# Kernel tuning notes

Hardware: AMD Instinct MI355X
Metric: run time of the kernel (lower is better)

The kernel has to match this reference:

```python
import jax, jax.numpy as jnp
import numpy as np

NEG_SLOPE = 0.2

def gat_conv(x, src, dst, n, W, a_src, a_dst, b):
    # PyG GATConv, heads=1: h = xW; e_ij = LeakyReLU(a_src.h_j + a_dst.h_i)
    # alpha = softmax over incoming edges of i; out_i = sum_j alpha_ij * h_j + b
    h = x @ W                               # [N, F_out]
    s_src = h @ a_src                       # [N]
    s_dst = h @ a_dst                       # [N]
    e = s_src[src] + s_dst[dst]             # [E]
    e = jnp.where(e > 0, e, NEG_SLOPE * e)  # leaky relu
    # numerically stable scatter-softmax over destination groups
    m = jax.ops.segment_max(e, dst, num_segments=n)          # [N]
    ee = jnp.exp(e - m[dst])                                  # [E]
    denom = jax.ops.segment_sum(ee, dst, num_segments=n)      # [N]
    alpha = ee / denom[dst]                                    # [E]
    out = jax.ops.segment_sum(alpha[:, None] * h[src], dst, num_segments=n)
    return out + b

def add_self_loops(edge_index, n):
    loops = jnp.arange(n, dtype=edge_index.dtype)
    src = jnp.concatenate([edge_index[0], loops])
    dst = jnp.concatenate([edge_index[1], loops])
    return src, dst

def setup_inputs() -> dict:
    key = jax.random.key(0)
    ks = jax.random.split(key, 12)
    N, E, F_IN, H1, H2, C = 50000, 800000, 1433, 512, 256, 7
    x = jax.random.normal(ks[0], (N, F_IN), dtype=jnp.float32)
    edge_index = jax.random.randint(ks[1], (2, E), 0, N, dtype=jnp.int64)
    def glorot(k, shape):
        lim = float(np.sqrt(6.0 / (shape[0] + shape[-1])))
        return jax.random.uniform(k, shape, jnp.float32, -lim, lim)
    params = {
        'W1': glorot(ks[2], (F_IN, H1)), 'as1': glorot(ks[3], (H1,)), 'ad1': glorot(ks[4], (H1,)), 'b1': jnp.zeros((H1,), jnp.float32),
        'W2': glorot(ks[5], (H1, H2)), 'as2': glorot(ks[6], (H2,)), 'ad2': glorot(ks[7], (H2,)), 'b2': jnp.zeros((H2,), jnp.float32),
        'W3': glorot(ks[8], (H2, C)), 'as3': glorot(ks[9], (C,)), 'ad3': glorot(ks[10], (C,)), 'b3': jnp.zeros((C,), jnp.float32),
    }
    return {'x': x, 'edge_index': edge_index, **params}

def reference(x, edge_index, W1, as1, ad1, b1, W2, as2, ad2, b2, W3, as3, ad3, b3):
    n = x.shape[0]
    src, dst = add_self_loops(edge_index, n)
    h = jax.nn.relu(gat_conv(x, src, dst, n, W1, as1, ad1, b1))
    h = jax.nn.relu(gat_conv(h, src, dst, n, W2, as2, ad2, b2))
    h = gat_conv(h, src, dst, n, W3, as3, ad3, b3)
    return jax.nn.log_softmax(h, axis=1)
```

## Files before the change

### kernel.cpp

```cpp
#include <hip/hip_runtime.h>
#include <hip/hip_bf16.h>
#include <math.h>

constexpr int N_NODES = 50000;
constexpr int E_EDGES = 800000;
constexpr int E_TOT   = E_EDGES + N_NODES;
constexpr int F_IN  = 1433;
constexpr int KPAD1 = 1440;
constexpr int F1 = 512;
constexpr int F2 = 256;
constexpr int NC = 7;
constexpr int MAXDEG = 1024;
constexpr float NEG_SLOPE = 0.2f;

typedef unsigned short u16;
typedef unsigned int   u32;
typedef short s16x8 __attribute__((ext_vector_type(8)));
typedef float f32x4 __attribute__((ext_vector_type(4)));
typedef float float4a __attribute__((ext_vector_type(4), aligned(4)));

__device__ inline u16 f2b(float f) {
    u32 u = __float_as_uint(f);
    u32 r = (u + 0x7fffu + ((u >> 16) & 1u)) >> 16;
    return (u16)r;
}
__device__ inline float b2f(u16 b) { return __uint_as_float(((u32)b) << 16); }

__device__ inline u32 pkbf16(float lo, float hi) {
    union { __hip_bfloat162 h; u32 u; } c;
    c.h = __float22bfloat162_rn(make_float2(lo, hi));
    return c.u;
}

__device__ inline void gload_lds16(const void* g, void* l) {
    __builtin_amdgcn_global_load_lds(
        (const __attribute__((address_space(1))) u32*)g,
        (__attribute__((address_space(3))) u32*)l, 16, 0, 0);
}

__global__ void count_dst_kernel(const int* __restrict__ dst, int* __restrict__ counts) {
    int i = blockIdx.x * blockDim.x + threadIdx.x;
    if (i < E_TOT) {
        int d = (i < E_EDGES) ? dst[i] : (i - E_EDGES);
        atomicAdd(&counts[d], 1);
    }
}

__global__ __launch_bounds__(1024) void scan_kernel(const int* __restrict__ counts,
                                                    int* __restrict__ row_ptr, int n) {
    __shared__ int part[1024];
    int t = threadIdx.x;
    int chunk = (n + 1023) / 1024;
    int lo = t * chunk;
    int hi = min(lo + chunk, n);
    int s = 0;
    for (int i = lo; i < hi; ++i) s += counts[i];
    part[t] = s;
    __syncthreads();
    for (int off = 1; off < 1024; off <<= 1) {
        int v = 0;
        if (t >= off) v = part[t - off];
        __syncthreads();
        part[t] += v;
        __syncthreads();
    }
    int run = part[t] - s;
    for (int i = lo; i < hi; ++i) { row_ptr[i] = run; run += counts[i]; }
    if (t == 1023) row_ptr[n] = part[1023];
}

__global__ void scatter_kernel(const int* __restrict__ src, const int* __restrict__ dst,
                               const int* __restrict__ row_ptr, int* __restrict__ fill,
                               int* __restrict__ col) {
    int i = blockIdx.x * blockDim.x + threadIdx.x;
    if (i < E_TOT) {
        int s = (i < E_EDGES) ? src[i] : (i - E_EDGES);
        int d = (i < E_EDGES) ? dst[i] : (i - E_EDGES);
        int p = row_ptr[d] + atomicAdd(&fill[d], 1);
        col[p] = s;
    }
}

__global__ void convert_wt_kernel(const float* __restrict__ W, u32* __restrict__ Wt,
                                  int K, int Nn, int KP) {
    int p = blockIdx.x * blockDim.x + threadIdx.x;
    int ppr = KP / 2;
    if (p >= Nn * ppr) return;
    int n = p / ppr;
    int k = (p - n * ppr) * 2;
    float v0 = (k + 0 < K) ? W[(size_t)(k + 0) * Nn + n] : 0.f;
    float v1 = (k + 1 < K) ? W[(size_t)(k + 1) * Nn + n] : 0.f;
    Wt[p] = (u32)f2b(v0) | ((u32)f2b(v1) << 16);
}

#define GEMM1_COMPUTE(P)                                                        \
    {                                                                           \
        const u16* sAc = &sA[(P) * ABUF];                                       \
        const u16* sBc = &sB[(P) * BBUF];                                       \
        s16x8 af[4], bf[8];                                                     \
        _Pragma("unroll")                                                       \
        for (int mt = 0; mt < 4; ++mt)                                          \
            af[mt] = *(const s16x8*)&sAc[(mt * 16 + lm) * 32 + rdoff];          \
        _Pragma("unroll")                                                       \
        for (int nt = 0; nt < 8; ++nt)                                          \
            bf[nt] = *(const s16x8*)&sBc[(wave * 128 + nt * 16 + lm) * 32 + rdoff]; \
        _Pragma("unroll")                                                       \
        for (int mt = 0; mt < 4; ++mt)                                          \
            _Pragma("unroll")                                                   \
            for (int nt = 0; nt < 8; ++nt)                                      \
                acc[mt][nt] = __builtin_amdgcn_mfma_f32_16x16x32_bf16(          \
                    af[mt], bf[nt], acc[mt][nt], 0, 0, 0);                      \
    }

#define GEMM1_BODY(i, P, Q)                                                     \
    {                                                                           \
        __builtin_amdgcn_s_barrier();                                           \
        int kA = ((i) + 2) * 32;                                                \
        aR0[P] = *(const float4a*)(xcol + kA);                                  \
        aR1[P] = *(const float4a*)(xcol + kA + 4);                              \
        int kB = ((i) + 1) * 32;                                                \
        _Pragma("unroll")                                                       \
        for (int c = 0; c < 8; ++c) gload_lds16(gB[c] + kB, lB[c] + (Q) * BBUF);\
        asm volatile("s_waitcnt vmcnt(10)" ::: "memory");                       \
        GEMM1_COMPUTE(P);                                                       \
        uint4 pk_;                                                              \
        pk_.x = pkbf16(aR0[Q][0], aR0[Q][1]);                                   \
        pk_.y = pkbf16(aR0[Q][2], aR0[Q][3]);                                   \
        pk_.z = pkbf16(aR1[Q][0], aR1[Q][1]);                                   \
        pk_.w = pkbf16(aR1[Q][2], aR1[Q][3]);                                   \
        *(uint4*)&sA[(Q) * ABUF + tid * 8] = pk_;                               \
        asm volatile("s_waitcnt lgkmcnt(0)" ::: "memory");                      \
    }

__global__ __launch_bounds__(256, 2) void gemm1_fused(const float* __restrict__ A,
                                                      const u16* __restrict__ Bt,
                                                      u16* __restrict__ C) {
    constexpr int M = N_NODES;
    constexpr int ABUF = 64 * 32;
    constexpr int BBUF = 512 * 32;
    __shared__ u16 sA[2 * ABUF];
    __shared__ u16 sB[2 * BBUF];
    int tid  = threadIdx.x;
    int wave = tid >> 6;
    int lane = tid & 63;
    int quad = lane >> 4;
    int lm   = lane & 15;
    int m0 = blockIdx.x * 64;

    int arow  = min(m0 + (tid >> 2), M - 1);
    int aslot = (tid & 3) ^ ((tid >> 3) & 3);
    const float* xcol = A + (size_t)arow * F_IN + aslot * 8;

    const u16* gB[8];
    u16* lB[8];
#pragma unroll
    for (int c = 0; c < 8; ++c) {
        int chunk = wave * 8 + c;
        int row  = chunk * 16 + (lane >> 2);
        int slot = (lane & 3) ^ ((lane >> 3) & 3);
        gB[c] = Bt + (size_t)row * KPAD1 + slot * 8;
        lB[c] = &sB[chunk * 512];
    }

    f32x4 acc[4][8];
#pragma unroll
    for (int i = 0; i < 4; ++i)
#pragma unroll
        for (int j = 0; j < 8; ++j) acc[i][j] = (f32x4){0.f, 0.f, 0.f, 0.f};

    int rdoff = (quad ^ ((lm >> 1) & 3)) * 8;

    float4a aR0[2], aR1[2];

    aR0[0] = *(const float4a*)(xcol + 0);
    aR1[0] = *(const float4a*)(xcol + 4);
    aR0[1] = *(const float4a*)(xcol + 32);
    aR1[1] = *(const float4a*)(xcol + 36);
#pragma unroll
    for (int c = 0; c < 8; ++c) gload_lds16(gB[c], lB[c]);
    asm volatile("s_waitcnt vmcnt(10)" ::: "memory");
    {
        uint4 pk_;
        pk_.x = pkbf16(aR0[0][0], aR0[0][1]);
        pk_.y = pkbf16(aR0[0][2], aR0[0][3]);
        pk_.z = pkbf16(aR1[0][0], aR1[0][1]);
        pk_.w = pkbf16(aR1[0][2], aR1[0][3]);
        *(uint4*)&sA[tid * 8] = pk_;
    }
    asm volatile("s_waitcnt lgkmcnt(0)" ::: "memory");

    for (int ii = 0; ii < 42; ii += 2) {
        GEMM1_BODY(ii, 0, 1);
        GEMM1_BODY(ii + 1, 1, 0);
    }

    __syncthreads();
    float tv[8];
    {
        int c0 = 1408 + aslot * 8;
#pragma unroll
        for (int q = 0; q < 8; ++q)
            tv[q] = (c0 + q < F_IN) ? xcol[1408 + q] : 0.f;
    }
#pragma unroll
    for (int c = 0; c < 8; ++c) gload_lds16(gB[c] + 43 * 32, lB[c] + BBUF);
    GEMM1_COMPUTE(0);
    {
        uint4 pk_;
        pk_.x = pkbf16(aR0[1][0], aR0[1][1]);
        pk_.y = pkbf16(aR0[1][2], aR0[1][3]);
        pk_.z = pkbf16(aR1[1][0], aR1[1][1]);
        pk_.w = pkbf16(aR1[1][2], aR1[1][3]);
        *(uint4*)&sA[ABUF + tid * 8] = pk_;
    }
    __syncthreads();
#pragma unroll
    for (int c = 0; c < 8; ++c) gload_lds16(gB[c] + 44 * 32, lB[c]);
    GEMM1_COMPUTE(1);
    {
        uint4 pk_;
        pk_.x = pkbf16(tv[0], tv[1]);
        pk_.y = pkbf16(tv[2], tv[3]);
        pk_.z = pkbf16(tv[4], tv[5]);
        pk_.w = pkbf16(tv[6], tv[7]);
        *(uint4*)&sA[tid * 8] = pk_;
    }
    __syncthreads();
    GEMM1_COMPUTE(0);

#pragma unroll
    for (int mt = 0; mt < 4; ++mt) {
        int mbase = m0 + mt * 16 + quad * 4;
#pragma unroll
        for (int nt = 0; nt < 8; ++nt) {
            int n = wave * 128 + nt * 16 + lm;
#pragma unroll
            for (int r = 0; r < 4; ++r) {
                int m = mbase + r;
                if (m < M) C[(size_t)m * F1 + n] = f2b(acc[mt][nt][r]);
            }
        }
    }
}

__global__ __launch_bounds__(256) void mfma_gemm_bt(const u16* __restrict__ A,
                                                    const u16* __restrict__ Bt,
                                                    u16* __restrict__ C,
                                                    int M, int N, int K) {
    __shared__ u16 sA[128 * 32];
    __shared__ u16 sB[128 * 32];
    int tid  = threadIdx.x;
    int wave = tid >> 6;
    int lane = tid & 63;
    int quad = lane >> 4;
    int lm   = lane & 15;
    int wm = wave & 1;
    int wn = wave >> 1;
    int m0 = blockIdx.y * 128;
    int n0 = blockIdx.x * 128;

    int ch0 = wave * 2, ch1 = wave * 2 + 1;
    int rsub = lane >> 2;
    int slot = (lane & 3) ^ ((lane >> 3) & 3);
    int csub = slot * 8;
    int ar0 = min(m0 + ch0 * 16 + rsub, M - 1);
    int ar1 = min(m0 + ch1 * 16 + rsub, M - 1);
    int br0 = n0 + ch0 * 16 + rsub;
    int br1 = n0 + ch1 * 16 + rsub;
    const u16* gA0 = A + (size_t)ar0 * K + csub;
    const u16* gA1 = A + (size_t)ar1 * K + csub;
    const u16* gB0 = Bt + (size_t)br0 * K + csub;
    const u16* gB1 = Bt + (size_t)br1 * K + csub;

    f32x4 acc[4][4];
#pragma unroll
    for (int i = 0; i < 4; ++i)
#pragma unroll
        for (int j = 0; j < 4; ++j) acc[i][j] = (f32x4){0.f, 0.f, 0.f, 0.f};

    int rdoff = (quad ^ ((lm >> 1) & 3)) * 8;

    for (int k0 = 0; k0 < K; k0 += 32) {
        gload_lds16(gA0 + k0, &sA[ch0 * 512]);
        gload_lds16(gA1 + k0, &sA[ch1 * 512]);
        gload_lds16(gB0 + k0, &sB[ch0 * 512]);
        gload_lds16(gB1 + k0, &sB[ch1 * 512]);
        __syncthreads();

        s16x8 af[4], bf[4];
#pragma unroll
        for (int mt = 0; mt < 4; ++mt)
            af[mt] = *(const s16x8*)&sA[(wm * 64 + mt * 16 + lm) * 32 + rdoff];
#pragma unroll
        for (int nt = 0; nt < 4; ++nt)
            bf[nt] = *(const s16x8*)&sB[(wn * 64 + nt * 16 + lm) * 32 + rdoff];
#pragma unroll
        for (int mt = 0; mt < 4; ++mt)
#pragma unroll
            for (int nt = 0; nt < 4; ++nt)
                acc[mt][nt] = __builtin_amdgcn_mfma_f32_16x16x32_bf16(
                    af[mt], bf[nt], acc[mt][nt], 0, 0, 0);
        __syncthreads();
    }

#pragma unroll
    for (int mt = 0; mt < 4; ++mt) {
        int mbase = m0 + wm * 64 + mt * 16 + quad * 4;
#pragma unroll
        for (int nt = 0; nt < 4; ++nt) {
            int n = n0 + wn * 64 + nt * 16 + lm;
#pragma unroll
            for (int r = 0; r < 4; ++r) {
                int m = mbase + r;
                if (m < M) C[(size_t)m * N + n] = f2b(acc[mt][nt][r]);
            }
        }
    }
}

template <int F>
__global__ __launch_bounds__(256) void scores_bf16_kernel(const u16* __restrict__ h,
                                                          const float* __restrict__ a_src,
                                                          const float* __restrict__ a_dst,
                                                          float* __restrict__ s_src,
                                                          float* __restrict__ s_dst, int n) {
    int gwid = (blockIdx.x * blockDim.x + threadIdx.x) >> 6;
    int lane = threadIdx.x & 63;
    if (gwid >= n) return;
    const u32* row = (const u32*)(h + (size_t)gwid * F);
    float acc1 = 0.f, acc2 = 0.f;
    for (int p = lane; p < F / 2; p += 64) {
        u32 u = row[p];
        float v0 = b2f((u16)(u & 0xffff));
        float v1 = b2f((u16)(u >> 16));
        acc1 += v0 * a_src[2 * p] + v1 * a_src[2 * p + 1];
        acc2 += v0 * a_dst[2 * p] + v1 * a_dst[2 * p + 1];
    }
#pragma unroll
    for (int o = 32; o; o >>= 1) {
        acc1 += __shfl_xor(acc1, o);
        acc2 += __shfl_xor(acc2, o);
    }
    if (lane == 0) { s_src[gwid] = acc1; s_dst[gwid] = acc2; }
}

template <int F>
__global__ __launch_bounds__(256) void scores_kernel(const float* __restrict__ h,
                                                     const float* __restrict__ a_src,
                                                     const float* __restrict__ a_dst,
                                                     float* __restrict__ s_src,
                                                     float* __restrict__ s_dst, int n) {
    int gwid = (blockIdx.x * blockDim.x + threadIdx.x) >> 6;
    int lane = threadIdx.x & 63;
    if (gwid >= n) return;
    const float* row = h + (size_t)gwid * F;
    float acc1 = 0.f, acc2 = 0.f;
    for (int f = lane; f < F; f += 64) {
        float v = row[f];
        acc1 += v * a_src[f];
        acc2 += v * a_dst[f];
    }
#pragma unroll
    for (int o = 32; o; o >>= 1) {
        acc1 += __shfl_xor(acc1, o);
        acc2 += __shfl_xor(acc2, o);
    }
    if (lane == 0) { s_src[gwid] = acc1; s_dst[gwid] = acc2; }
}

template <int F, bool OUT_BF16>
__global__ __launch_bounds__(256) void agg_online_kernel(
        const u16* __restrict__ h, const float* __restrict__ s_src,
        const float* __restrict__ s_dst, const float* __restrict__ bias,
        const int* __restrict__ row_ptr, const int* __restrict__ col,
        void* __restrict__ out, int n) {
    constexpr int UPL = F / 128;
    int gwid = (blockIdx.x * blockDim.x + threadIdx.x) >> 6;
    int lane = threadIdx.x & 63;
    if (gwid >= n) return;
    int beg = row_ptr[gwid];
    int end = row_ptr[gwid + 1];
    float sd = s_dst[gwid];
    const u32* hw = (const u32*)h;
    int loff = lane * UPL;

    float m = -1e30f, denom = 0.f;
    float acc[2 * UPL];
#pragma unroll
    for (int e = 0; e < 2 * UPL; ++e) acc[e] = 0.f;

    int j = beg;
    for (; j + 2 <= end; j += 2) {
        int c0 = col[j], c1 = col[j + 1];
        const u32* r0 = hw + (size_t)c0 * (F / 2) + loff;
        const u32* r1 = hw + (size_t)c1 * (F / 2) + loff;
        u32 v0[UPL], v1[UPL];
        if constexpr (UPL == 4) {
            uint4 q0 = *(const uint4*)r0; v0[0]=q0.x; v0[1]=q0.y; v0[2]=q0.z; v0[3]=q0.w;
            uint4 q1 = *(const uint4*)r1; v1[0]=q1.x; v1[1]=q1.y; v1[2]=q1.z; v1[3]=q1.w;
        } else {
            uint2 q0 = *(const uint2*)r0; v0[0]=q0.x; v0[1]=q0.y;
            uint2 q1 = *(const uint2*)r1; v1[0]=q1.x; v1[1]=q1.y;
        }
        float e0 = s_src[c0] + sd; e0 = (e0 > 0.f) ? e0 : NEG_SLOPE * e0;
        float e1 = s_src[c1] + sd; e1 = (e1 > 0.f) ? e1 : NEG_SLOPE * e1;
        float mn = fmaxf(fmaxf(m, e0), e1);
        float sc = expf(m - mn);
        float w0 = expf(e0 - mn);
        float w1 = expf(e1 - mn);
        denom = denom * sc + w0 + w1;
        m = mn;
#pragma unroll
        for (int u = 0; u < UPL; ++u) {
            acc[2*u]   = acc[2*u]   * sc + w0 * b2f((u16)(v0[u] & 0xffff))
                                         + w1 * b2f((u16)(v1[u] & 0xffff));
            acc[2*u+1] = acc[2*u+1] * sc + w0 * b2f((u16)(v0[u] >> 16))
                                         + w1 * b2f((u16)(v1[u] >> 16));
        }
    }
    if (j < end) {
        int c0 = col[j];
        const u32* r0 = hw + (size_t)c0 * (F / 2) + loff;
        u32 v0[UPL];
        if constexpr (UPL == 4) {
            uint4 q0 = *(const uint4*)r0; v0[0]=q0.x; v0[1]=q0.y; v0[2]=q0.z; v0[3]=q0.w;
        } else {
            uint2 q0 = *(const uint2*)r0; v0[0]=q0.x; v0[1]=q0.y;
        }
        float e0 = s_src[c0] + sd; e0 = (e0 > 0.f) ? e0 : NEG_SLOPE * e0;
        float mn = fmaxf(m, e0);
        float sc = expf(m - mn);
        float w0 = expf(e0 - mn);
        denom = denom * sc + w0;
        m = mn;
#pragma unroll
        for (int u = 0; u < UPL; ++u) {
            acc[2*u]   = acc[2*u]   * sc + w0 * b2f((u16)(v0[u] & 0xffff));
            acc[2*u+1] = acc[2*u+1] * sc + w0 * b2f((u16)(v0[u] >> 16));
        }
    }

    float inv = 1.0f / denom;
    if constexpr (OUT_BF16) {
        const float2* bp2 = (const float2*)bias;
        u32 ov[UPL];
#pragma unroll
        for (int u = 0; u < UPL; ++u) {
            float2 bb = bp2[loff + u];
            float v0 = fmaxf(acc[2*u]   * inv + bb.x, 0.f);
            float v1 = fmaxf(acc[2*u+1] * inv + bb.y, 0.f);
            ov[u] = pkbf16(v0, v1);
        }
        u32* op = (u32*)out + (size_t)gwid * (F / 2) + loff;
        if constexpr (UPL == 4) {
            uint4 q = {ov[0], ov[1], ov[2], ov[3]};
            *(uint4*)op = q;
        } else {
            uint2 q = {ov[0], ov[1]};
            *(uint2*)op = q;
        }
    } else {
        const float* bp = bias + 2 * loff;
        float4 q = { fmaxf(acc[0] * inv + bp[0], 0.f),
                     fmaxf(acc[1] * inv + bp[1], 0.f),
                     fmaxf(acc[2] * inv + bp[2], 0.f),
                     fmaxf(acc[3] * inv + bp[3], 0.f) };
        *(float4*)((float*)out + (size_t)gwid * F + 2 * loff) = q;
    }
}

__global__ __launch_bounds__(64) void agg_lsm7_kernel(const float* __restrict__ h,
                                                      const float* __restrict__ s_src,
                                                      const float* __restrict__ s_dst,
                                                      const float* __restrict__ bias,
                                                      const int* __restrict__ row_ptr,
                                                      const int* __restrict__ col,
                                                      float* __restrict__ out) {
    int node = blockIdx.x;
    int lane = threadIdx.x;
    int beg = row_ptr[node];
    int deg = min(row_ptr[node + 1] - beg, MAXDEG);

    __shared__ float w[MAXDEG];
    __shared__ int cs[MAXDEG];

    float sd = s_dst[node];
    float m = -1e30f;
    for (int j = lane; j < deg; j += 64) {
        int s = col[beg + j];
        cs[j] = s;
        float e = s_src[s] + sd;
        e = (e > 0.f) ? e : NEG_SLOPE * e;
        w[j] = e;
        m = fmaxf(m, e);
    }
#pragma unroll
    for (int o = 32; o; o >>= 1) m = fmaxf(m, __shfl_xor(m, o));
    float sum = 0.f;
    for (int j = lane; j < deg; j += 64) {
        float v = expf(w[j] - m);
        w[j] = v;
        sum += v;
    }
#pragma unroll
    for (int o = 32; o; o >>= 1) sum += __shfl_xor(sum, o);
    float inv = 1.0f / sum;

    float a[NC];
#pragma unroll
    for (int f = 0; f < NC; ++f) a[f] = 0.f;
    for (int j = lane; j < deg; j += 64) {
        float wg = w[j] * inv;
        const float* row = h + (size_t)cs[j] * NC;
#pragma unroll
        for (int f = 0; f < NC; ++f) a[f] += wg * row[f];
    }
#pragma unroll
    for (int f = 0; f < NC; ++f)
#pragma unroll
        for (int o = 32; o; o >>= 1) a[f] += __shfl_xor(a[f], o);

    if (lane == 0) {
        float vals[NC];
        float mx = -1e30f;
#pragma unroll
        for (int f = 0; f < NC; ++f) { vals[f] = a[f] + bias[f]; mx = fmaxf(mx, vals[f]); }
        float ssum = 0.f;
#pragma unroll
        for (int f = 0; f < NC; ++f) ssum += expf(vals[f] - mx);
        float lse = mx + logf(ssum);
#pragma unroll
        for (int f = 0; f < NC; ++f) out[(size_t)node * NC + f] = vals[f] - lse;
    }
}

__global__ __launch_bounds__(256) void gemm3_kernel(const float* __restrict__ A,
                                                    const float* __restrict__ W,
                                                    float* __restrict__ out, int n) {
    __shared__ float sW[F2 * NC];
    for (int i = threadIdx.x; i < F2 * NC; i += blockDim.x) sW[i] = W[i];
    __syncthreads();
    int gwid = (blockIdx.x * blockDim.x + threadIdx.x) >> 6;
    int lane = threadIdx.x & 63;
    if (gwid >= n) return;
    const float* row = A + (size_t)gwid * F2;
    float4 v = *(const float4*)(row + lane * 4);
    float res = 0.f;
#pragma unroll
    for (int c = 0; c < NC; ++c) {
        float p = v.x * sW[(lane * 4 + 0) * NC + c] + v.y * sW[(lane * 4 + 1) * NC + c] +
                  v.z * sW[(lane * 4 + 2) * NC + c] + v.w * sW[(lane * 4 + 3) * NC + c];
#pragma unroll
        for (int o = 32; o; o >>= 1) p += __shfl_xor(p, o);
        if (lane == c) res = p;
    }
    if (lane < NC) out[(size_t)gwid * NC + lane] = res;
}

extern "C" void kernel_launch(void* const* d_in, const int* in_sizes, int n_in,
                              void* d_out, int out_size, void* d_ws, size_t ws_size,
                              hipStream_t stream) {
    const float* x   = (const float*)d_in[0];
    const int* ei    = (const int*)d_in[1];
    const int* src   = ei;
    const int* dst   = ei + E_EDGES;
    const float* W1  = (const float*)d_in[2];
    const float* as1 = (const float*)d_in[3];
    const float* ad1 = (const float*)d_in[4];
    const float* b1  = (const float*)d_in[5];
    const float* W2  = (const float*)d_in[6];
    const float* as2 = (const float*)d_in[7];
    const float* ad2 = (const float*)d_in[8];
    const float* b2  = (const float*)d_in[9];
    const float* W3  = (const float*)d_in[10];
    const float* as3 = (const float*)d_in[11];
    const float* ad3 = (const float*)d_in[12];
    const float* b3  = (const float*)d_in[13];
    float* outp = (float*)d_out;

    char* base = (char*)d_ws;
    u16*  a1b = (u16*)base;
    u16*  h2b = (u16*)(base + 51200000);
    float* a2 = (float*)(base + 76800000);
    float* h3 = (float*)(base + 128000000);
    u16*  h1b = (u16*)(base + 144000000);
    u16*  W1t = (u16*)(base + 195200000);
    u16*  W2t = (u16*)(base + 196674560);
    float* ssrc = (float*)(base + 196936704);
    float* sdst = (float*)(base + 197136704);
    int* row_ptr = (int*)(base + 197336704);
    int* counts  = (int*)(base + 197536708);
    int* fill    = (int*)(base + 197736708);
    int* col     = (int*)(base + 197936708);

    hipMemsetAsync(counts, 0, sizeof(int) * N_NODES, stream);
    hipMemsetAsync(fill, 0, sizeof(int) * N_NODES, stream);

    {
        int blk = 256;
        int grid = (E_TOT + blk - 1) / blk;
        count_dst_kernel<<<grid, blk, 0, stream>>>(dst, counts);
        scan_kernel<<<1, 1024, 0, stream>>>(counts, row_ptr, N_NODES);
        scatter_kernel<<<grid, blk, 0, stream>>>(src, dst, row_ptr, fill, col);
    }

    {
        int nw1 = F1 * (KPAD1 / 2);
        convert_wt_kernel<<<(nw1 + 255) / 256, 256, 0, stream>>>(W1, (u32*)W1t, F_IN, F1, KPAD1);
        int nw2 = F2 * (F1 / 2);
        convert_wt_kernel<<<(nw2 + 255) / 256, 256, 0, stream>>>(W2, (u32*)W2t, F1, F2, F1);
    }

    int waves_grid = (N_NODES + 3) / 4;
    int mblocks = (N_NODES + 127) / 128;

    {
        int grid1 = (N_NODES + 63) / 64;
        gemm1_fused<<<grid1, 256, 0, stream>>>(x, W1t, h1b);
        scores_bf16_kernel<F1><<<waves_grid, 256, 0, stream>>>(h1b, as1, ad1, ssrc, sdst, N_NODES);
        agg_online_kernel<F1, true><<<waves_grid, 256, 0, stream>>>(
            h1b, ssrc, sdst, b1, row_ptr, col, a1b, N_NODES);
    }
    {
        dim3 grid(F2 / 128, mblocks);
        mfma_gemm_bt<<<grid, 256, 0, stream>>>(a1b, W2t, h2b, N_NODES, F2, F1);
        scores_bf16_kernel<F2><<<waves_grid, 256, 0, stream>>>(h2b, as2, ad2, ssrc, sdst, N_NODES);
        agg_online_kernel<F2, false><<<waves_grid, 256, 0, stream>>>(
            h2b, ssrc, sdst, b2, row_ptr, col, a2, N_NODES);
    }
    {
        gemm3_kernel<<<waves_grid, 256, 0, stream>>>(a2, W3, h3, N_NODES);
        scores_kernel<NC><<<waves_grid, 256, 0, stream>>>(h3, as3, ad3, ssrc, sdst, N_NODES);
        agg_lsm7_kernel<<<N_NODES, 64, 0, stream>>>(
            h3, ssrc, sdst, b3, row_ptr, col, outp);
    }
}
```

Before: 1.039 ms.

## Simplify gemm1 pipeline to a single-stage double buffer with nontemporal loads

```diff
diff --git a/kernel.cpp b/kernel.cpp
--- a/kernel.cpp
+++ b/kernel.cpp
@@ -36,6 +36,18 @@
     __builtin_amdgcn_global_load_lds(
         (const __attribute__((address_space(1))) u32*)g,
         (__attribute__((address_space(3))) u32*)l, 16, 0, 0);
+}
+
+__device__ inline void loadA8_nt(const float* p, int gk, float4a& v0, float4a& v1) {
+    if (gk + 8 <= F_IN) {
+        v0 = __builtin_nontemporal_load((const float4a*)p);
+        v1 = __builtin_nontemporal_load((const float4a*)(p + 4));
+    } else {
+#pragma unroll
+        for (int i = 0; i < 4; ++i) v0[i] = (gk + i < F_IN) ? p[i] : 0.f;
+#pragma unroll
+        for (int i = 0; i < 4; ++i) v1[i] = (gk + 4 + i < F_IN) ? p[4 + i] : 0.f;
+    }
 }
 
 __global__ void count_dst_kernel(const int* __restrict__ dst, int* __restrict__ counts) {
@@ -93,45 +105,6 @@
     Wt[p] = (u32)f2b(v0) | ((u32)f2b(v1) << 16);
 }
 
-#define GEMM1_COMPUTE(P)                                                        \
-    {                                                                           \
-        const u16* sAc = &sA[(P) * ABUF];                                       \
-        const u16* sBc = &sB[(P) * BBUF];                                       \
-        s16x8 af[4], bf[8];                                                     \
-        _Pragma("unroll")                                                       \
-        for (int mt = 0; mt < 4; ++mt)                                          \
-            af[mt] = *(const s16x8*)&sAc[(mt * 16 + lm) * 32 + rdoff];          \
-        _Pragma("unroll")                                                       \
-        for (int nt = 0; nt < 8; ++nt)                                          \
-            bf[nt] = *(const s16x8*)&sBc[(wave * 128 + nt * 16 + lm) * 32 + rdoff]; \
-        _Pragma("unroll")                                                       \
-        for (int mt = 0; mt < 4; ++mt)                                          \
-            _Pragma("unroll")                                                   \
-            for (int nt = 0; nt < 8; ++nt)                                      \
-                acc[mt][nt] = __builtin_amdgcn_mfma_f32_16x16x32_bf16(          \
-                    af[mt], bf[nt], acc[mt][nt], 0, 0, 0);                      \
-    }
-
-#define GEMM1_BODY(i, P, Q)                                                     \
-    {                                                                           \
-        __builtin_amdgcn_s_barrier();                                           \
-        int kA = ((i) + 2) * 32;                                                \
-        aR0[P] = *(const float4a*)(xcol + kA);                                  \
-        aR1[P] = *(const float4a*)(xcol + kA + 4);                              \
-        int kB = ((i) + 1) * 32;                                                \
-        _Pragma("unroll")                                                       \
-        for (int c = 0; c < 8; ++c) gload_lds16(gB[c] + kB, lB[c] + (Q) * BBUF);\
-        asm volatile("s_waitcnt vmcnt(10)" ::: "memory");                       \
-        GEMM1_COMPUTE(P);                                                       \
-        uint4 pk_;                                                              \
-        pk_.x = pkbf16(aR0[Q][0], aR0[Q][1]);                                   \
-        pk_.y = pkbf16(aR0[Q][2], aR0[Q][3]);                                   \
-        pk_.z = pkbf16(aR1[Q][0], aR1[Q][1]);                                   \
-        pk_.w = pkbf16(aR1[Q][2], aR1[Q][3]);                                   \
-        *(uint4*)&sA[(Q) * ABUF + tid * 8] = pk_;                               \
-        asm volatile("s_waitcnt lgkmcnt(0)" ::: "memory");                      \
-    }
-
 __global__ __launch_bounds__(256, 2) void gemm1_fused(const float* __restrict__ A,
                                                       const u16* __restrict__ Bt,
                                                       u16* __restrict__ C) {
@@ -150,6 +123,7 @@
     int arow  = min(m0 + (tid >> 2), M - 1);
     int aslot = (tid & 3) ^ ((tid >> 3) & 3);
     const float* xcol = A + (size_t)arow * F_IN + aslot * 8;
+    int acolbase = aslot * 8;
 
     const u16* gB[8];
     u16* lB[8];
@@ -170,63 +144,56 @@
 
     int rdoff = (quad ^ ((lm >> 1) & 3)) * 8;
 
-    float4a aR0[2], aR1[2];
-
-    aR0[0] = *(const float4a*)(xcol + 0);
-    aR1[0] = *(const float4a*)(xcol + 4);
-    aR0[1] = *(const float4a*)(xcol + 32);
-    aR1[1] = *(const float4a*)(xcol + 36);
-#pragma unroll
-    for (int c = 0; c < 8; ++c) gload_lds16(gB[c], lB[c]);
-    asm volatile("s_waitcnt vmcnt(10)" ::: "memory");
     {
-        uint4 pk_;
-        pk_.x = pkbf16(aR0[0][0], aR0[0][1]);
-        pk_.y = pkbf16(aR0[0][2], aR0[0][3]);
-        pk_.z = pkbf16(aR1[0][0], aR1[0][1]);
-        pk_.w = pkbf16(aR1[0][2], aR1[0][3]);
-        *(uint4*)&sA[tid * 8] = pk_;
-    }
-    asm volatile("s_waitcnt lgkmcnt(0)" ::: "memory");
-
-    for (int ii = 0; ii < 42; ii += 2) {
-        GEMM1_BODY(ii, 0, 1);
-        GEMM1_BODY(ii + 1, 1, 0);
-    }
-
+#pragma unroll
+        for (int c = 0; c < 8; ++c) gload_lds16(gB[c], lB[c]);
+        float4a a0, a1;
+        loadA8_nt(xcol, acolbase, a0, a1);
+        uint4 pk;
+        pk.x = pkbf16(a0[0], a0[1]); pk.y = pkbf16(a0[2], a0[3]);
+        pk.z = pkbf16(a1[0], a1[1]); pk.w = pkbf16(a1[2], a1[3]);
+        *(uint4*)&sA[tid * 8] = pk;
+    }
     __syncthreads();
-    float tv[8];
-    {
-        int c0 = 1408 + aslot * 8;
-#pragma unroll
-        for (int q = 0; q < 8; ++q)
-            tv[q] = (c0 + q < F_IN) ? xcol[1408 + q] : 0.f;
-    }
-#pragma unroll
-    for (int c = 0; c < 8; ++c) gload_lds16(gB[c] + 43 * 32, lB[c] + BBUF);
-    GEMM1_COMPUTE(0);
-    {
-        uint4 pk_;
-        pk_.x = pkbf16(aR0[1][0], aR0[1][1]);
-        pk_.y = pkbf16(aR0[1][2], aR0[1][3]);
-        pk_.z = pkbf16(aR1[1][0], aR1[1][1]);
-        pk_.w = pkbf16(aR1[1][2], aR1[1][3]);
-        *(uint4*)&sA[ABUF + tid * 8] = pk_;
-    }
-    __syncthreads();
-#pragma unroll
-    for (int c = 0; c < 8; ++c) gload_lds16(gB[c] + 44 * 32, lB[c]);
-    GEMM1_COMPUTE(1);
-    {
-        uint4 pk_;
-        pk_.x = pkbf16(tv[0], tv[1]);
-        pk_.y = pkbf16(tv[2], tv[3]);
-        pk_.z = pkbf16(tv[4], tv[5]);
-        pk_.w = pkbf16(tv[6], tv[7]);
-        *(uint4*)&sA[tid * 8] = pk_;
-    }
-    __syncthreads();
-    GEMM1_COMPUTE(0);
+
+    int cur = 0;
+    for (int k0 = 0; k0 < KPAD1; k0 += 32) {
+        int kn = k0 + 32;
+        bool hasnext = kn < KPAD1;
+        int nxt = cur ^ 1;
+
+        float4a a0, a1;
+        if (hasnext) {
+#pragma unroll
+            for (int c = 0; c < 8; ++c) gload_lds16(gB[c] + kn, lB[c] + nxt * BBUF);
+            loadA8_nt(xcol + kn, acolbase + kn, a0, a1);
+        }
+
+        const u16* sAc = &sA[cur * ABUF];
+        const u16* sBc = &sB[cur * BBUF];
+        s16x8 af[4], bf[8];
+#pragma unroll
+        for (int mt = 0; mt < 4; ++mt)
+            af[mt] = *(const s16x8*)&sAc[(mt * 16 + lm) * 32 + rdoff];
+#pragma unroll
+        for (int nt = 0; nt < 8; ++nt)
+            bf[nt] = *(const s16x8*)&sBc[(wave * 128 + nt * 16 + lm) * 32 + rdoff];
+#pragma unroll
+        for (int mt = 0; mt < 4; ++mt)
+#pragma unroll
+            for (int nt = 0; nt < 8; ++nt)
+                acc[mt][nt] = __builtin_amdgcn_mfma_f32_16x16x32_bf16(
+                    af[mt], bf[nt], acc[mt][nt], 0, 0, 0);
+
+        if (hasnext) {
+            uint4 pk;
+            pk.x = pkbf16(a0[0], a0[1]); pk.y = pkbf16(a0[2], a0[3]);
+            pk.z = pkbf16(a1[0], a1[1]); pk.w = pkbf16(a1[2], a1[3]);
+            *(uint4*)&sA[nxt * ABUF + tid * 8] = pk;
+        }
+        __syncthreads();
+        cur = nxt;
+    }
 
 #pragma unroll
     for (int mt = 0; mt < 4; ++mt) {
@@ -237,7 +204,9 @@
 #pragma unroll
             for (int r = 0; r < 4; ++r) {
                 int m = mbase + r;
-                if (m < M) C[(size_t)m * F1 + n] = f2b(acc[mt][nt][r]);
+                if (m < M)
+                    __builtin_nontemporal_store(f2b(acc[mt][nt][r]),
+                                                &C[(size_t)m * F1 + n]);
             }
         }
     }
```

Result: no change. 1.056 ms (+1.7%).
